# Kernel tuning notes

Hardware: AMD Instinct MI355X
Metric: run time of the kernel (lower is better)

The kernel has to match this reference:

```python
import jax, jax.numpy as jnp
import numpy as np

EPS = 1e-5

def _bn(x, g, b, m, v):
    # inference-mode BatchNorm over channel axis 1
    shp = [1] * x.ndim
    shp[1] = x.shape[1]
    return (x - m.reshape(shp)) * (g.reshape(shp) / jnp.sqrt(v.reshape(shp) + EPS)) + b.reshape(shp)

def _forward(x, wdr, bdr, g1, be1, m1, v1, g2, be2, m2, v2, wrow, brow, wfc, bfc,
             wdrs, bdrs, g3, be3, m3, v3, g4, be4, m4, v4, wrows, brows, wfcs, bfcs):
    B, C, H, W = x.shape
    r = jax.nn.relu(x)

    # ---- channel attention (chan_att) ----
    y = jnp.einsum('bchw,oc->bohw', r, wdr) + bdr[None, :, None, None]   # 1x1 conv DR
    y = jax.nn.relu(_bn(y, g1, be1, m1, v1))
    Bc, D, _, _ = y.shape
    M = H * W
    yf = y.reshape(B, D, M)
    yc = yf - yf.mean(axis=2, keepdims=True)
    cov = jnp.einsum('bcm,bdm->bcd', yc, yc) / M                         # MPNCOV CovpoolLayer: x I_hat x^T, [B,D,D]
    cov = _bn(cov, g2, be2, m2, v2)                                      # row_bn (channel axis = D)
    # grouped conv: per-channel i, 4 filters over row i -> [B, D, 4]
    vch = jnp.einsum('bik,ijk->bij', cov, wrow).reshape(B, -1) + brow    # [B, 4D]
    catt = jax.nn.sigmoid(vch @ wfc.T + bfc)                             # fc_adapt_channels -> [B, C]
    catt = catt[:, :, None, None]

    # ---- spatial attention (pos_att) ----
    s = jnp.einsum('bchw,oc->bohw', r, wdrs) + bdrs[None, :, None, None]
    s = _bn(s, g3, be3, m3, v3)
    fh, fw = H // 8, W // 8
    sp = s.reshape(B, D, 8, fh, 8, fw).mean(axis=(3, 5))                 # adaptive avg pool -> 8x8
    M2 = 64
    sf = sp.reshape(B, D, M2)
    # cov_feature: x^T I_hat x with I_hat = (1/M2)(I_D - (1/M2) J_D)
    colsum = sf.sum(axis=1)                                              # [B, 64]
    covs = (jnp.einsum('bcm,bcn->bmn', sf, sf)
            - colsum[:, :, None] * colsum[:, None, :] / M2) / M2         # [B,64,64]
    covs = _bn(covs, g4, be4, m4, v4)
    vs = jnp.einsum('bik,ijk->bij', covs, wrows).reshape(B, -1) + brows  # [B,256]
    vs = jax.nn.relu(vs)
    patt = jax.nn.sigmoid(vs @ wfcs.T + bfcs)                            # [B,64]
    patt = patt.reshape(B, 1, 8, 8)
    patt = jnp.repeat(jnp.repeat(patt, fh, axis=2), fw, axis=3)          # adaptive unpool (exact replication)

    # attention == '+'
    return x * catt + jax.nn.relu(x * patt)

def setup_inputs() -> dict:
    key = jax.random.key(0)
    ks = jax.random.split(key, 32)
    B, C, H, W, D = 32, 512, 56, 56, 128
    n = lambda k, s, sc: jax.random.normal(k, s, dtype=jnp.float32) * sc
    u = lambda k, s: jax.random.uniform(k, s, dtype=jnp.float32)
    inp = {
        'x': n(ks[0], (B, C, H, W), 1.0),
        'wdr': n(ks[1], (D, C), 0.04), 'bdr': n(ks[2], (D,), 0.02),
        'g1': u(ks[3], (D,)) + 0.5, 'be1': n(ks[4], (D,), 0.1), 'm1': n(ks[5], (D,), 0.1), 'v1': u(ks[6], (D,)) * 0.5 + 0.5,
        'g2': u(ks[7], (D,)) + 0.5, 'be2': n(ks[8], (D,), 0.1), 'm2': n(ks[9], (D,), 0.1), 'v2': u(ks[10], (D,)) * 0.5 + 0.5,
        'wrow': n(ks[11], (D, 4, D), 0.08), 'brow': n(ks[12], (4 * D,), 0.02),
        'wfc': n(ks[13], (C, 4 * D), 0.04), 'bfc': n(ks[14], (C,), 0.02),
        'wdrs': n(ks[15], (D, C), 0.04), 'bdrs': n(ks[16], (D,), 0.02),
        'g3': u(ks[17], (D,)) + 0.5, 'be3': n(ks[18], (D,), 0.1), 'm3': n(ks[19], (D,), 0.1), 'v3': u(ks[20], (D,)) * 0.5 + 0.5,
        'g4': u(ks[21], (64,)) + 0.5, 'be4': n(ks[22], (64,), 0.1), 'm4': n(ks[23], (64,), 0.1), 'v4': u(ks[24], (64,)) * 0.5 + 0.5,
        'wrows': n(ks[25], (64, 4, 64), 0.1), 'brows': n(ks[26], (256,), 0.02),
        'wfcs': n(ks[27], (64, 256), 0.06), 'bfcs': n(ks[28], (64,), 0.02),
    }
    return inp

def reference(x, wdr, bdr, g1, be1, m1, v1, g2, be2, m2, v2, wrow, brow, wfc, bfc,
              wdrs, bdrs, g3, be3, m3, v3, g4, be4, m4, v4, wrows, brows, wfcs, bfcs):
    return _forward(x, wdr, bdr, g1, be1, m1, v1, g2, be2, m2, v2, wrow, brow, wfc, bfc,
                    wdrs, bdrs, g3, be3, m3, v3, g4, be4, m4, v4, wrows, brows, wfcs, bfcs)
```

## Files before the change

kernel.cpp:

```cpp
#include <hip/hip_runtime.h>
#include <hip/hip_bf16.h>

#define EPS 1e-5f

typedef short bf16x8 __attribute__((ext_vector_type(8)));
typedef float f32x4  __attribute__((ext_vector_type(4)));
typedef float f32x4n __attribute__((ext_vector_type(4)));

union BF8 { ushort u[8]; bf16x8 v; };

__device__ __forceinline__ ushort f2bf(float f) {
  uint u = __float_as_uint(f);
  u += 0x7fffu + ((u >> 16) & 1u);
  return (ushort)(u >> 16);
}
__device__ __forceinline__ float bf2f(ushort u) {
  return __uint_as_float(((uint)u) << 16);
}
__device__ __forceinline__ f32x4 mfma16(bf16x8 a, bf16x8 b, f32x4 c) {
  return __builtin_amdgcn_mfma_f32_16x16x32_bf16(a, b, c, 0, 0, 0);
}

__global__ __launch_bounds__(256) void k_zero(float4* __restrict__ p) {
  p[blockIdx.x * 256 + threadIdx.x] = make_float4(0.f, 0.f, 0.f, 0.f);
}

__global__ __launch_bounds__(256) void k_prep(
    const float* __restrict__ wdr, const float* __restrict__ wdrs,
    const float* __restrict__ bdr,
    const float* __restrict__ g1, const float* __restrict__ be1,
    const float* __restrict__ m1, const float* __restrict__ v1,
    const float* __restrict__ wfc,
    ushort* __restrict__ wdr_bf, ushort* __restrict__ wdrs_bf,
    float* __restrict__ sc1, float* __restrict__ sh1,
    float* __restrict__ wfcT) {
  int i = blockIdx.x * 256 + threadIdx.x;
  if (i < 65536) {
    wdr_bf[i]  = f2bf(wdr[i]);
    wdrs_bf[i] = f2bf(wdrs[i] * (1.0f / 49.0f));
  }
  if (i < 262144) {
    int c = i >> 9, p = i & 511;
    wfcT[p * 512 + c] = wfc[i];
  }
  if (i < 128) {
    float a = g1[i] / sqrtf(v1[i] + EPS);
    sc1[i] = a;
    sh1[i] = (bdr[i] - m1[i]) * a + be1[i];
  }
}

__global__ __launch_bounds__(256) void k_convy(
    const float* __restrict__ x, const ushort* __restrict__ wdr_bf,
    const float* __restrict__ sc1, const float* __restrict__ sh1,
    ushort* __restrict__ y_bf, float* __restrict__ rp) {
  __shared__ ushort xs[9216];
  __shared__ float pool[1024];
  __shared__ float sc_s[128], sh_s[128];

  const int t  = threadIdx.x;
  const int b  = blockIdx.y;
  const int n0 = blockIdx.x * 128;

  if (t < 128) { sc_s[t] = sc1[t]; sh_s[t] = sh1[t]; }
  pool[t] = 0.f; pool[t + 256] = 0.f; pool[t + 512] = 0.f; pool[t + 768] = 0.f;

  const int cl = t & 7;
  const int nq = t >> 3;
  const int nl = nq * 4;
  const int ng = n0 + nl;
  const bool nv = ng < 3136;
  const int h   = ng / 56;
  const int w   = ng - h * 56;
  const int gh0 = (n0 / 56) / 7;
  const int lb0 = (h / 7 - gh0) * 8 + (w / 7);
  const int lb3 = (h / 7 - gh0) * 8 + ((w + 3) / 7);
  int split = 7 - (w % 7); if (split > 4) split = 4;
  const int ng8  = nq >> 1;
  const int nsub = (nq & 1) * 4;

  const int l  = t & 63;
  const int wv = t >> 6;
  const int wr = wv >> 1, wc = wv & 1;
  const int lm = l & 15,  lk = l >> 4;

  f32x4 acc[4][4];
#pragma unroll
  for (int a = 0; a < 4; a++)
#pragma unroll
    for (int c = 0; c < 4; c++) acc[a][c] = (f32x4){0.f, 0.f, 0.f, 0.f};

  __syncthreads();

  for (int kc = 0; kc < 8; kc++) {
#pragma unroll
    for (int r = 0; r < 8; r++) {
      int cc = r * 8 + cl;
      int c  = kc * 64 + cc;
      float4 v4 = make_float4(0.f, 0.f, 0.f, 0.f);
      if (nv) v4 = *(const float4*)(x + ((size_t)(b * 512 + c)) * 3136 + ng);
      float e0 = fmaxf(v4.x, 0.f), e1 = fmaxf(v4.y, 0.f);
      float e2 = fmaxf(v4.z, 0.f), e3 = fmaxf(v4.w, 0.f);
      if (nv) {
        float s0 = e0, s1 = 0.f;
        if (split > 1) s0 += e1; else s1 += e1;
        if (split > 2) s0 += e2; else s1 += e2;
        if (split > 3) s0 += e3; else s1 += e3;
        atomicAdd(&pool[cc * 16 + lb0], s0);
        if (lb3 != lb0) atomicAdd(&pool[cc * 16 + lb3], s1);
      }
      int base = (cc >> 3) * 1152 + ng8 * 72 + nsub * 8 + (cc & 7);
      xs[base]      = f2bf(e0);
      xs[base + 8]  = f2bf(e1);
      xs[base + 16] = f2bf(e2);
      xs[base + 24] = f2bf(e3);
    }
    __syncthreads();

#pragma unroll
    for (int ki = 0; ki < 2; ki++) {
      bf16x8 af[4], bfr[4];
#pragma unroll
      for (int mi = 0; mi < 4; mi++) {
        int m = wr * 64 + mi * 16 + lm;
        af[mi] = *(const bf16x8*)(wdr_bf + m * 512 + kc * 64 + ki * 32 + lk * 8);
      }
#pragma unroll
      for (int ni = 0; ni < 4; ni++) {
        int n = wc * 64 + ni * 16 + lm;
        int a = (ki * 4 + lk) * 1152 + (n >> 3) * 72 + (n & 7) * 8;
        bfr[ni] = *(const bf16x8*)(xs + a);
      }
#pragma unroll
      for (int mi = 0; mi < 4; mi++)
#pragma unroll
        for (int ni = 0; ni < 4; ni++)
          acc[mi][ni] = mfma16(af[mi], bfr[ni], acc[mi][ni]);
    }

#pragma unroll
    for (int f = 0; f < 4; f++) {
      int idx = t + f * 256;
      float pv = pool[idx];
      int cL = idx >> 4, lb = idx & 15;
      int gbin = gh0 * 8 + lb;
      if (pv != 0.f && gbin < 64)
        atomicAdd(&rp[((size_t)(b * 64 + gbin)) * 512 + kc * 64 + cL], pv);
      pool[idx] = 0.f;
    }
    __syncthreads();
  }

#pragma unroll
  for (int mi = 0; mi < 4; mi++) {
#pragma unroll
    for (int ni = 0; ni < 4; ni++) {
      int n_g = n0 + wc * 64 + ni * 16 + lm;
      if (n_g >= 3136) continue;
#pragma unroll
      for (int r = 0; r < 4; r++) {
        int m = wr * 64 + mi * 16 + lk * 4 + r;
        float v = acc[mi][ni][r] * sc_s[m] + sh_s[m];
        v = fmaxf(v, 0.f);
        y_bf[((size_t)(b * 128 + m)) * 3136 + n_g] = f2bf(v);
      }
    }
  }
}

__global__ __launch_bounds__(256) void k_gram(
    const ushort* __restrict__ y_bf, float* __restrict__ G, float* __restrict__ S) {
  __shared__ ushort ys[128 * 40];
  const int t  = threadIdx.x;
  const int b  = blockIdx.y;
  const int k0 = blockIdx.x * 448;

  const int l  = t & 63, wv = t >> 6;
  const int wr = wv >> 1, wc = wv & 1;
  const int lm = l & 15,  lk = l >> 4;

  const int mA = t >> 2, k8 = t & 3;

  f32x4 acc[4][4];
#pragma unroll
  for (int a = 0; a < 4; a++)
#pragma unroll
    for (int c = 0; c < 4; c++) acc[a][c] = (f32x4){0.f, 0.f, 0.f, 0.f};
  float sA = 0.f, sB = 0.f;

  for (int kc = 0; kc < 14; kc++) {
    int kk = k0 + kc * 32;
    BF8 v0, v1;
    v0.v = *(const bf16x8*)(y_bf + ((size_t)(b * 128 + mA)) * 3136 + kk + k8 * 8);
    v1.v = *(const bf16x8*)(y_bf + ((size_t)(b * 128 + mA + 64)) * 3136 + kk + k8 * 8);
#pragma unroll
    for (int j = 0; j < 8; j++) { sA += bf2f(v0.u[j]); sB += bf2f(v1.u[j]); }
    *(bf16x8*)(ys + mA * 40 + k8 * 8) = v0.v;
    *(bf16x8*)(ys + (mA + 64) * 40 + k8 * 8) = v1.v;
    __syncthreads();

    bf16x8 af[4], bfr[4];
#pragma unroll
    for (int mi = 0; mi < 4; mi++)
      af[mi] = *(const bf16x8*)(ys + (wr * 64 + mi * 16 + lm) * 40 + lk * 8);
#pragma unroll
    for (int ni = 0; ni < 4; ni++)
      bfr[ni] = *(const bf16x8*)(ys + (wc * 64 + ni * 16 + lm) * 40 + lk * 8);
#pragma unroll
    for (int mi = 0; mi < 4; mi++)
#pragma unroll
      for (int ni = 0; ni < 4; ni++)
        acc[mi][ni] = mfma16(af[mi], bfr[ni], acc[mi][ni]);
    __syncthreads();
  }

#pragma unroll
  for (int mi = 0; mi < 4; mi++)
#pragma unroll
    for (int ni = 0; ni < 4; ni++)
#pragma unroll
      for (int r = 0; r < 4; r++) {
        int i = wr * 64 + mi * 16 + lk * 4 + r;
        int j = wc * 64 + ni * 16 + lm;
        atomicAdd(&G[((size_t)(b * 128 + i)) * 128 + j], acc[mi][ni][r]);
      }
  atomicAdd(&S[b * 128 + mA], sA);
  atomicAdd(&S[b * 128 + mA + 64], sB);
}

__global__ __launch_bounds__(256) void k_catt(
    const float* __restrict__ G, const float* __restrict__ S,
    const float* __restrict__ g2, const float* __restrict__ be2,
    const float* __restrict__ m2, const float* __restrict__ v2,
    const float* __restrict__ wrow, const float* __restrict__ brow,
    const float* __restrict__ wfcT, const float* __restrict__ bfc,
    float* __restrict__ catt) {
  __shared__ float Ss[128];
  __shared__ float vch_s[512];
  const int t = threadIdx.x;
  const int b = blockIdx.x;
  const float invM = 1.0f / 3136.0f;
  if (t < 128) Ss[t] = S[b * 128 + t];
  __syncthreads();
#pragma unroll
  for (int rep = 0; rep < 2; rep++) {
    int p = t + rep * 256;
    int i = p >> 2, j = p & 3;
    float a2  = g2[i] / sqrtf(v2[i] + EPS);
    float mi2 = m2[i], bei = be2[i];
    float Si  = Ss[i] * invM;
    const float* Grow = G + ((size_t)(b * 128 + i)) * 128;
    const float* wr_  = wrow + (i * 4 + j) * 128;
    float a = 0.f;
    for (int k = 0; k < 128; k++) {
      float cov = (Grow[k] - Si * Ss[k]) * invM;
      a += ((cov - mi2) * a2 + bei) * wr_[k];
    }
    vch_s[p] = a + brow[p];
  }
  __syncthreads();
#pragma unroll
  for (int rep = 0; rep < 2; rep++) {
    int c = t + rep * 256;
    float z = bfc[c];
    for (int p = 0; p < 512; p++) z += vch_s[p] * wfcT[p * 512 + c];
    catt[b * 512 + c] = 1.f / (1.f + expf(-z));
  }
}

__global__ __launch_bounds__(256) void k_sconv(
    const float* __restrict__ rp, const ushort* __restrict__ wdrs_bf,
    const float* __restrict__ bdrs,
    const float* __restrict__ g3, const float* __restrict__ be3,
    const float* __restrict__ m3, const float* __restrict__ v3,
    ushort* __restrict__ sfT) {
  const int t = threadIdx.x;
  const int b = blockIdx.x;
  const int l = t & 63, wv = t >> 6;
  const int wm = wv >> 1, wn = wv & 1;
  const int lm = l & 15,  lk = l >> 4;
  f32x4 acc[4][2];
#pragma unroll
  for (int a = 0; a < 4; a++) { acc[a][0] = (f32x4){0.f,0.f,0.f,0.f}; acc[a][1] = (f32x4){0.f,0.f,0.f,0.f}; }

  for (int kk = 0; kk < 16; kk++) {
    bf16x8 af[4], bfr[2];
#pragma unroll
    for (int mi = 0; mi < 4; mi++) {
      int m = wm * 64 + mi * 16 + lm;
      af[mi] = *(const bf16x8*)(wdrs_bf + m * 512 + kk * 32 + lk * 8);
    }
#pragma unroll
    for (int ni = 0; ni < 2; ni++) {
      int g = wn * 32 + ni * 16 + lm;
      const float* pb = rp + ((size_t)(b * 64 + g)) * 512 + kk * 32 + lk * 8;
      float4 fa = *(const float4*)pb;
      float4 fb = *(const float4*)(pb + 4);
      BF8 bb;
      bb.u[0] = f2bf(fa.x); bb.u[1] = f2bf(fa.y); bb.u[2] = f2bf(fa.z); bb.u[3] = f2bf(fa.w);
      bb.u[4] = f2bf(fb.x); bb.u[5] = f2bf(fb.y); bb.u[6] = f2bf(fb.z); bb.u[7] = f2bf(fb.w);
      bfr[ni] = bb.v;
    }
#pragma unroll
    for (int mi = 0; mi < 4; mi++)
#pragma unroll
      for (int ni = 0; ni < 2; ni++)
        acc[mi][ni] = mfma16(af[mi], bfr[ni], acc[mi][ni]);
  }
#pragma unroll
  for (int mi = 0; mi < 4; mi++)
#pragma unroll
    for (int ni = 0; ni < 2; ni++) {
      int g = wn * 32 + ni * 16 + lm;
#pragma unroll
      for (int r = 0; r < 4; r++) {
        int d = wm * 64 + mi * 16 + lk * 4 + r;
        float a3 = g3[d] / sqrtf(v3[d] + EPS);
        float sf = (acc[mi][ni][r] + bdrs[d] - m3[d]) * a3 + be3[d];
        sfT[((size_t)(b * 64 + g)) * 128 + d] = f2bf(sf);
      }
    }
}

__global__ __launch_bounds__(256) void k_patt(
    const ushort* __restrict__ sfT,
    const float* __restrict__ g4, const float* __restrict__ be4,
    const float* __restrict__ m4, const float* __restrict__ v4,
    const float* __restrict__ wrows, const float* __restrict__ brows,
    const float* __restrict__ wfcs, const float* __restrict__ bfcs,
    float* __restrict__ patt) {
  __shared__ float colsum_s[64];
  __shared__ float covbn_s[64 * 65];
  __shared__ float vs_s[256];
  const int t = threadIdx.x;
  const int b = blockIdx.x;
  if (t < 64) {
    float cs = 0.f;
    const ushort* row = sfT + ((size_t)(b * 64 + t)) * 128;
    for (int dq = 0; dq < 16; dq++) {
      BF8 v; v.v = *(const bf16x8*)(row + dq * 8);
#pragma unroll
      for (int j = 0; j < 8; j++) cs += bf2f(v.u[j]);
    }
    colsum_s[t] = cs;
  }
  __syncthreads();

  const int l = t & 63, wv = t >> 6;
  const int wr = wv >> 1, wc = wv & 1;
  const int lm = l & 15,  lk = l >> 4;
  f32x4 acc[2][2];
  acc[0][0] = (f32x4){0.f,0.f,0.f,0.f}; acc[0][1] = (f32x4){0.f,0.f,0.f,0.f};
  acc[1][0] = (f32x4){0.f,0.f,0.f,0.f}; acc[1][1] = (f32x4){0.f,0.f,0.f,0.f};
  for (int kk = 0; kk < 4; kk++) {
    bf16x8 af[2], bfr[2];
#pragma unroll
    for (int mi = 0; mi < 2; mi++)
      af[mi] = *(const bf16x8*)(sfT + ((size_t)(b * 64 + wr * 32 + mi * 16 + lm)) * 128 + kk * 32 + lk * 8);
#pragma unroll
    for (int ni = 0; ni < 2; ni++)
      bfr[ni] = *(const bf16x8*)(sfT + ((size_t)(b * 64 + wc * 32 + ni * 16 + lm)) * 128 + kk * 32 + lk * 8);
#pragma unroll
    for (int mi = 0; mi < 2; mi++)
#pragma unroll
      for (int ni = 0; ni < 2; ni++)
        acc[mi][ni] = mfma16(af[mi], bfr[ni], acc[mi][ni]);
  }
  const float inv64 = 1.0f / 64.0f;
#pragma unroll
  for (int mi = 0; mi < 2; mi++)
#pragma unroll
    for (int ni = 0; ni < 2; ni++) {
      int j = wc * 32 + ni * 16 + lm;
#pragma unroll
      for (int r = 0; r < 4; r++) {
        int i = wr * 32 + mi * 16 + lk * 4 + r;
        float cv = (acc[mi][ni][r] - colsum_s[i] * colsum_s[j] * inv64) * inv64;
        float a4 = g4[i] / sqrtf(v4[i] + EPS);
        covbn_s[i * 65 + j] = (cv - m4[i]) * a4 + be4[i];
      }
    }
  __syncthreads();
  {
    int m = t >> 2, j = t & 3;
    float a = brows[t];
    const float* wr_ = wrows + (m * 4 + j) * 64;
    for (int k = 0; k < 64; k++) a += covbn_s[m * 65 + k] * wr_[k];
    vs_s[t] = fmaxf(a, 0.f);
  }
  __syncthreads();
  if (t < 64) {
    float z = bfcs[t];
    const float* wf = wfcs + t * 256;
    for (int p = 0; p < 256; p++) z += vs_s[p] * wf[p];
    patt[b * 64 + t] = 1.f / (1.f + expf(-z));
  }
}

__global__ __launch_bounds__(256) void k_final(
    const float* __restrict__ x, const float* __restrict__ catt,
    const float* __restrict__ patt, float* __restrict__ out) {
  int gi = blockIdx.x * 256 + threadIdx.x;
  int bc = gi / 784;
  int q  = gi - bc * 784;
  int n  = q * 4;
  int b  = bc >> 9;
  float ca = catt[bc];
  int h = n / 56;
  int w = n - h * 56;
  const float* pp = patt + b * 64 + (h / 7) * 8;
  float p0 = pp[w / 7], p1 = pp[(w + 1) / 7], p2 = pp[(w + 2) / 7], p3 = pp[(w + 3) / 7];
  float4 xv = *(const float4*)(x + (size_t)gi * 4);
  float4 o;
  o.x = xv.x * ca + fmaxf(xv.x * p0, 0.f);
  o.y = xv.y * ca + fmaxf(xv.y * p1, 0.f);
  o.z = xv.z * ca + fmaxf(xv.z * p2, 0.f);
  o.w = xv.w * ca + fmaxf(xv.w * p3, 0.f);
  *(float4*)(out + (size_t)gi * 4) = o;
}

extern "C" void kernel_launch(void* const* d_in, const int* in_sizes, int n_in,
                              void* d_out, int out_size, void* d_ws, size_t ws_size,
                              hipStream_t stream) {
  const float* x     = (const float*)d_in[0];
  const float* wdr   = (const float*)d_in[1];
  const float* bdr   = (const float*)d_in[2];
  const float* g1    = (const float*)d_in[3];
  const float* be1   = (const float*)d_in[4];
  const float* m1    = (const float*)d_in[5];
  const float* v1    = (const float*)d_in[6];
  const float* g2    = (const float*)d_in[7];
  const float* be2   = (const float*)d_in[8];
  const float* m2    = (const float*)d_in[9];
  const float* v2    = (const float*)d_in[10];
  const float* wrow  = (const float*)d_in[11];
  const float* brow  = (const float*)d_in[12];
  const float* wfc   = (const float*)d_in[13];
  const float* bfc   = (const float*)d_in[14];
  const float* wdrs  = (const float*)d_in[15];
  const float* bdrs  = (const float*)d_in[16];
  const float* g3    = (const float*)d_in[17];
  const float* be3   = (const float*)d_in[18];
  const float* m3    = (const float*)d_in[19];
  const float* v3    = (const float*)d_in[20];
  const float* g4    = (const float*)d_in[21];
  const float* be4   = (const float*)d_in[22];
  const float* m4    = (const float*)d_in[23];
  const float* v4    = (const float*)d_in[24];
  const float* wrows = (const float*)d_in[25];
  const float* brows = (const float*)d_in[26];
  const float* wfcs  = (const float*)d_in[27];
  const float* bfcs  = (const float*)d_in[28];

  char* ob = (char*)d_out;
  ushort* y_bf    = (ushort*)(ob + 0x0000000);
  ushort* wdr_bf  = (ushort*)(ob + 0x2000000);
  ushort* wdrs_bf = (ushort*)(ob + 0x2020000);
  float*  sc1     = (float*) (ob + 0x2040000);
  float*  sh1     = (float*) (ob + 0x2040200);
  float*  wfcT    = (float*) (ob + 0x2050000);
  float*  rp      = (float*) (ob + 0x2150000);
  float*  G       = (float*) (ob + 0x2550000);
  float*  S       = (float*) (ob + 0x2750000);
  float*  sfTf    = (float*) (ob + 0x2760000);
  ushort* sfT     = (ushort*)(ob + 0x2760000);
  (void)sfTf;

  char* ws = (char*)d_ws;
  float* catt = (float*)(ws + 0x00000);
  float* patt = (float*)(ws + 0x10000);

  k_zero<<<1540, 256, 0, stream>>>((float4*)(ob + 0x2150000));

  k_prep<<<1024, 256, 0, stream>>>(wdr, wdrs, bdr, g1, be1, m1, v1, wfc,
                                   wdr_bf, wdrs_bf, sc1, sh1, wfcT);
  k_convy<<<dim3(25, 32), 256, 0, stream>>>(x, wdr_bf, sc1, sh1, y_bf, rp);
  k_gram<<<dim3(7, 32), 256, 0, stream>>>(y_bf, G, S);
  k_catt<<<32, 256, 0, stream>>>(G, S, g2, be2, m2, v2, wrow, brow, wfcT, bfc, catt);
  k_sconv<<<32, 256, 0, stream>>>(rp, wdrs_bf, bdrs, g3, be3, m3, v3, sfT);
  k_patt<<<32, 256, 0, stream>>>(sfT, g4, be4, m4, v4, wrows, brows, wfcs, bfcs, patt);
  k_final<<<50176, 256, 0, stream>>>(x, catt, patt, (float*)d_out);
}
```

Measured before the change: 654.3 us.

## Double-buffer LDS and prefetch global loads in conv and gram kernels

In k_convy and k_gram, the next chunk of global data is now loaded into registers while the current chunk is processed. Shared-memory staging and pooling buffers are double-buffered, which removes the second __syncthreads per iteration. The goal is to hide global load latency and cut barrier cost. In exchange it adds register pressure from the extra float4/bf16 staging arrays, which could lower occupancy, and doubles LDS use.

```diff
diff --git a/kernel.cpp b/kernel.cpp
--- a/kernel.cpp
+++ b/kernel.cpp
@@ -5,7 +5,6 @@
 
 typedef short bf16x8 __attribute__((ext_vector_type(8)));
 typedef float f32x4  __attribute__((ext_vector_type(4)));
-typedef float f32x4n __attribute__((ext_vector_type(4)));
 
 union BF8 { ushort u[8]; bf16x8 v; };
 
@@ -54,8 +53,8 @@
     const float* __restrict__ x, const ushort* __restrict__ wdr_bf,
     const float* __restrict__ sc1, const float* __restrict__ sh1,
     ushort* __restrict__ y_bf, float* __restrict__ rp) {
-  __shared__ ushort xs[9216];
-  __shared__ float pool[1024];
+  __shared__ ushort xs[2][9216];
+  __shared__ float pool[2][1024];
   __shared__ float sc_s[128], sh_s[128];
 
   const int t  = threadIdx.x;
@@ -63,7 +62,8 @@
   const int n0 = blockIdx.x * 128;
 
   if (t < 128) { sc_s[t] = sc1[t]; sh_s[t] = sh1[t]; }
-  pool[t] = 0.f; pool[t + 256] = 0.f; pool[t + 512] = 0.f; pool[t + 768] = 0.f;
+#pragma unroll
+  for (int f = 0; f < 4; f++) { pool[0][t + f * 256] = 0.f; pool[1][t + f * 256] = 0.f; }
 
   const int cl = t & 7;
   const int nq = t >> 3;
@@ -84,36 +84,54 @@
   const int wr = wv >> 1, wc = wv & 1;
   const int lm = l & 15,  lk = l >> 4;
 
+  const float* xb = x + (size_t)(b * 512) * 3136 + ng;
+
   f32x4 acc[4][4];
 #pragma unroll
   for (int a = 0; a < 4; a++)
 #pragma unroll
     for (int c = 0; c < 4; c++) acc[a][c] = (f32x4){0.f, 0.f, 0.f, 0.f};
 
+  const float4 z4 = make_float4(0.f, 0.f, 0.f, 0.f);
+  float4 rA[8], rB[8];
+
+#pragma unroll
+  for (int r = 0; r < 8; r++) {
+    rA[r] = z4;
+    if (nv) rA[r] = *(const float4*)(xb + (size_t)(r * 8 + cl) * 3136);
+  }
+
   __syncthreads();
 
   for (int kc = 0; kc < 8; kc++) {
+    if (kc < 7) {
+#pragma unroll
+      for (int r = 0; r < 8; r++) {
+        rB[r] = z4;
+        if (nv) rB[r] = *(const float4*)(xb + (size_t)((kc + 1) * 64 + r * 8 + cl) * 3136);
+      }
+    }
+
+    ushort* xsb = xs[kc & 1];
+    float*  plb = pool[kc & 1];
 #pragma unroll
     for (int r = 0; r < 8; r++) {
       int cc = r * 8 + cl;
-      int c  = kc * 64 + cc;
-      float4 v4 = make_float4(0.f, 0.f, 0.f, 0.f);
-      if (nv) v4 = *(const float4*)(x + ((size_t)(b * 512 + c)) * 3136 + ng);
-      float e0 = fmaxf(v4.x, 0.f), e1 = fmaxf(v4.y, 0.f);
-      float e2 = fmaxf(v4.z, 0.f), e3 = fmaxf(v4.w, 0.f);
+      float e0 = fmaxf(rA[r].x, 0.f), e1 = fmaxf(rA[r].y, 0.f);
+      float e2 = fmaxf(rA[r].z, 0.f), e3 = fmaxf(rA[r].w, 0.f);
       if (nv) {
         float s0 = e0, s1 = 0.f;
         if (split > 1) s0 += e1; else s1 += e1;
         if (split > 2) s0 += e2; else s1 += e2;
         if (split > 3) s0 += e3; else s1 += e3;
-        atomicAdd(&pool[cc * 16 + lb0], s0);
-        if (lb3 != lb0) atomicAdd(&pool[cc * 16 + lb3], s1);
+        atomicAdd(&plb[cc * 16 + lb0], s0);
+        if (lb3 != lb0) atomicAdd(&plb[cc * 16 + lb3], s1);
       }
       int base = (cc >> 3) * 1152 + ng8 * 72 + nsub * 8 + (cc & 7);
-      xs[base]      = f2bf(e0);
-      xs[base + 8]  = f2bf(e1);
-      xs[base + 16] = f2bf(e2);
-      xs[base + 24] = f2bf(e3);
+      xsb[base]      = f2bf(e0);
+      xsb[base + 8]  = f2bf(e1);
+      xsb[base + 16] = f2bf(e2);
+      xsb[base + 24] = f2bf(e3);
     }
     __syncthreads();
 
@@ -129,7 +147,7 @@
       for (int ni = 0; ni < 4; ni++) {
         int n = wc * 64 + ni * 16 + lm;
         int a = (ki * 4 + lk) * 1152 + (n >> 3) * 72 + (n & 7) * 8;
-        bfr[ni] = *(const bf16x8*)(xs + a);
+        bfr[ni] = *(const bf16x8*)(xsb + a);
       }
 #pragma unroll
       for (int mi = 0; mi < 4; mi++)
@@ -141,14 +159,18 @@
 #pragma unroll
     for (int f = 0; f < 4; f++) {
       int idx = t + f * 256;
-      float pv = pool[idx];
+      float pv = plb[idx];
       int cL = idx >> 4, lb = idx & 15;
       int gbin = gh0 * 8 + lb;
       if (pv != 0.f && gbin < 64)
         atomicAdd(&rp[((size_t)(b * 64 + gbin)) * 512 + kc * 64 + cL], pv);
-      pool[idx] = 0.f;
-    }
-    __syncthreads();
+      plb[idx] = 0.f;
+    }
+
+    if (kc < 7) {
+#pragma unroll
+      for (int r = 0; r < 8; r++) rA[r] = rB[r];
+    }
   }
 
 #pragma unroll
@@ -170,7 +192,7 @@
 
 __global__ __launch_bounds__(256) void k_gram(
     const ushort* __restrict__ y_bf, float* __restrict__ G, float* __restrict__ S) {
-  __shared__ ushort ys[128 * 40];
+  __shared__ ushort ys[2][128 * 40];
   const int t  = threadIdx.x;
   const int b  = blockIdx.y;
   const int k0 = blockIdx.x * 448;
@@ -180,6 +202,8 @@
   const int lm = l & 15,  lk = l >> 4;
 
   const int mA = t >> 2, k8 = t & 3;
+  const ushort* yb = y_bf + ((size_t)(b * 128 + mA)) * 3136 + k0 + k8 * 8;
+  const size_t rowoff = (size_t)64 * 3136;
 
   f32x4 acc[4][4];
 #pragma unroll
@@ -188,30 +212,36 @@
     for (int c = 0; c < 4; c++) acc[a][c] = (f32x4){0.f, 0.f, 0.f, 0.f};
   float sA = 0.f, sB = 0.f;
 
+  BF8 a0, a1, b0, b1;
+  a0.v = *(const bf16x8*)(yb);
+  a1.v = *(const bf16x8*)(yb + rowoff);
+
   for (int kc = 0; kc < 14; kc++) {
-    int kk = k0 + kc * 32;
-    BF8 v0, v1;
-    v0.v = *(const bf16x8*)(y_bf + ((size_t)(b * 128 + mA)) * 3136 + kk + k8 * 8);
-    v1.v = *(const bf16x8*)(y_bf + ((size_t)(b * 128 + mA + 64)) * 3136 + kk + k8 * 8);
-#pragma unroll
-    for (int j = 0; j < 8; j++) { sA += bf2f(v0.u[j]); sB += bf2f(v1.u[j]); }
-    *(bf16x8*)(ys + mA * 40 + k8 * 8) = v0.v;
-    *(bf16x8*)(ys + (mA + 64) * 40 + k8 * 8) = v1.v;
+    if (kc < 13) {
+      b0.v = *(const bf16x8*)(yb + (kc + 1) * 32);
+      b1.v = *(const bf16x8*)(yb + rowoff + (kc + 1) * 32);
+    }
+#pragma unroll
+    for (int j = 0; j < 8; j++) { sA += bf2f(a0.u[j]); sB += bf2f(a1.u[j]); }
+    ushort* ysb = ys[kc & 1];
+    *(bf16x8*)(ysb + mA * 40 + k8 * 8) = a0.v;
+    *(bf16x8*)(ysb + (mA + 64) * 40 + k8 * 8) = a1.v;
     __syncthreads();
 
     bf16x8 af[4], bfr[4];
 #pragma unroll
     for (int mi = 0; mi < 4; mi++)
-      af[mi] = *(const bf16x8*)(ys + (wr * 64 + mi * 16 + lm) * 40 + lk * 8);
+      af[mi] = *(const bf16x8*)(ysb + (wr * 64 + mi * 16 + lm) * 40 + lk * 8);
 #pragma unroll
     for (int ni = 0; ni < 4; ni++)
-      bfr[ni] = *(const bf16x8*)(ys + (wc * 64 + ni * 16 + lm) * 40 + lk * 8);
+      bfr[ni] = *(const bf16x8*)(ysb + (wc * 64 + ni * 16 + lm) * 40 + lk * 8);
 #pragma unroll
     for (int mi = 0; mi < 4; mi++)
 #pragma unroll
       for (int ni = 0; ni < 4; ni++)
         acc[mi][ni] = mfma16(af[mi], bfr[ni], acc[mi][ni]);
-    __syncthreads();
+
+    if (kc < 13) { a0 = b0; a1 = b1; }
   }
 
 #pragma unroll
@@ -462,9 +492,7 @@
   float*  rp      = (float*) (ob + 0x2150000);
   float*  G       = (float*) (ob + 0x2550000);
   float*  S       = (float*) (ob + 0x2750000);
-  float*  sfTf    = (float*) (ob + 0x2760000);
   ushort* sfT     = (ushort*)(ob + 0x2760000);
-  (void)sfTf;
 
   char* ws = (char*)d_ws;
   float* catt = (float*)(ws + 0x00000);
```

New measurement: 633.0 us. -3.3%, faster.
